# Performance work log

Measured on AMD Instinct MI355X. Metric: run time of the kernel, lower is better.

The kernel has to match this reference:

```python
import jax, jax.numpy as jnp
import numpy as np

N = 100000      # nodes
E = 1600000     # directed edges (before self loops)
IN, H, OUT = 16, 64, 8
NEG_SLOPE = 0.2  # PyG GATConv default


def setup_inputs() -> dict:
    key = jax.random.key(0)
    ks = jax.random.split(key, 12)
    g = lambda k, sh, s: (jax.random.normal(k, sh, dtype=jnp.float32) * s)
    return {
        "x": jax.random.normal(ks[0], (N, IN), dtype=jnp.float32),
        "edge_index": jax.random.randint(ks[1], (2, E), 0, N, dtype=jnp.int32),
        # layer 1 (GATConv: weight, att_src, att_dst, bias)
        "W1": g(ks[2], (IN, H), 1.0 / np.sqrt(IN)),
        "a_src1": g(ks[3], (H,), 0.1),
        "a_dst1": g(ks[4], (H,), 0.1),
        "b1": jnp.zeros((H,), jnp.float32),
        # layer 2
        "W2": g(ks[5], (H, H), 1.0 / np.sqrt(H)),
        "a_src2": g(ks[6], (H,), 0.1),
        "a_dst2": g(ks[7], (H,), 0.1),
        "b2": jnp.zeros((H,), jnp.float32),
        # policy head
        "Wp": g(ks[8], (H, OUT), 1.0 / np.sqrt(H)),
        "bp": jnp.zeros((OUT,), jnp.float32),
    }


def gat_conv(x, src, dst, W, a_src, a_dst, b):
    """PyG GATConv, heads=1: softmax over incoming edges grouped by dst."""
    h = x @ W                                   # [N, H]
    e = (h @ a_src)[src] + (h @ a_dst)[dst]      # [E'] raw attention logits
    e = jnp.where(e > 0, e, NEG_SLOPE * e)       # leaky_relu
    m = jax.ops.segment_max(e, dst, num_segments=N)
    m = jnp.where(jnp.isfinite(m), m, 0.0)       # guard empty segments
    w = jnp.exp(e - m[dst])
    den = jax.ops.segment_sum(w, dst, num_segments=N)
    alpha = w / (den[dst] + 1e-16)               # per-edge softmax weight
    out = jax.ops.segment_sum(h[src] * alpha[:, None], dst, num_segments=N)
    return out + b


def reference(x, edge_index, W1, a_src1, a_dst1, b1, W2, a_src2, a_dst2, b2, Wp, bp):
    # add self loops once (PyG default add_self_loops=True)
    loops = jnp.arange(N, dtype=edge_index.dtype)
    src = jnp.concatenate([edge_index[0], loops])
    dst = jnp.concatenate([edge_index[1], loops])
    h = jax.nn.relu(gat_conv(x, src, dst, W1, a_src1, a_dst1, b1))
    h = jax.nn.relu(gat_conv(h, src, dst, W2, a_src2, a_dst2, b2))
    return h @ Wp + bp  # [N, OUT]
```

## Files before the change

### kernel.cpp

```cpp
#include <hip/hip_runtime.h>
#include <hip/hip_fp16.h>
#include <math.h>

#define NEG_SLOPE 0.2f
#define TILE 2048

__device__ __forceinline__ float wave_reduce_sum(float v){
  #pragma unroll
  for (int off = 32; off > 0; off >>= 1) v += __shfl_xor(v, off, 64);
  return v;
}
__device__ __forceinline__ float wave_reduce_max(float v){
  #pragma unroll
  for (int off = 32; off > 0; off >>= 1) v = fmaxf(v, __shfl_xor(v, off, 64));
  return v;
}


__global__ void k_bcount(const int* __restrict__ ei, int* __restrict__ C,
                         int* __restrict__ Btot, int E, int TOT, int NB, int T){
  __shared__ int hist[512];
  int t = blockIdx.x;
  for (int i = threadIdx.x; i < NB; i += blockDim.x) hist[i] = 0;
  __syncthreads();
  int base = t * TILE;
  for (int k = threadIdx.x; k < TILE; k += blockDim.x){
    int j = base + k;
    if (j < TOT){
      int d = (j < E) ? ei[E + j] : (j - E);
      atomicAdd(&hist[d >> 8], 1);
    }
  }
  __syncthreads();
  for (int b = threadIdx.x; b < NB; b += blockDim.x){
    int v = hist[b];
    C[(size_t)b * T + t] = v;
    if (v) atomicAdd(&Btot[b], v);
  }
}

__global__ void k_bstart(const int* __restrict__ Btot, int* __restrict__ Bstart,
                         int* __restrict__ rowptr, int NB, int TOT, int N){
  __shared__ int lds[512];
  int t = threadIdx.x;
  int total = (t < NB) ? Btot[t] : 0;
  lds[t] = total; __syncthreads();
  for (int off = 1; off < 512; off <<= 1){
    int x = (t >= off) ? lds[t - off] : 0;
    __syncthreads();
    lds[t] += x;
    __syncthreads();
  }
  if (t < NB) Bstart[t] = lds[t] - total;
  if (t == 0){ Bstart[NB] = TOT; rowptr[N] = TOT; }
}

__global__ void k_bcolscan(const int* __restrict__ C, const int* __restrict__ Bstart,
                           int* __restrict__ O, int NB, int T){
  int wid = (blockIdx.x * blockDim.x + threadIdx.x) >> 6;
  int lane = threadIdx.x & 63;
  if (wid >= NB) return;
  int run = Bstart[wid];
  int nchunks = (T + 63) / 64;
  for (int i = 0; i < nchunks; i++){
    int t = i * 64 + lane;
    int v = (t < T) ? C[(size_t)wid * T + t] : 0;
    int s = v;
    #pragma unroll
    for (int off = 1; off < 64; off <<= 1){
      int u = __shfl_up(s, off);
      if (lane >= off) s += u;
    }
    if (t < T) O[(size_t)wid * T + t] = run + (s - v);
    run += __shfl(s, 63);
  }
}

__global__ void k_bscatter(const int* __restrict__ ei, const int* __restrict__ O,
                           unsigned int* __restrict__ tmp, int E, int TOT, int NB, int T){
  __shared__ int cur[512];
  int t = blockIdx.x;
  for (int b = threadIdx.x; b < NB; b += blockDim.x) cur[b] = O[(size_t)b * T + t];
  __syncthreads();
  int base = t * TILE;
  for (int k = threadIdx.x; k < TILE; k += blockDim.x){
    int j = base + k;
    if (j < TOT){
      int s, d;
      if (j < E){ s = ei[j]; d = ei[E + j]; } else { s = j - E; d = s; }
      int r = atomicAdd(&cur[d >> 8], 1);
      tmp[r] = ((unsigned)s << 8) | (unsigned)(d & 255);
    }
  }
}

__global__ void k_bfinal(const unsigned int* __restrict__ tmp, const int* __restrict__ Bstart,
                         int* __restrict__ rowptr, int* __restrict__ col, int N){
  __shared__ int hist[256];
  __shared__ int sc[256];
  __shared__ int cur[256];
  int b = blockIdx.x;
  int base_node = b << 8;
  int nnode = min(256, N - base_node);
  int beg = Bstart[b], end = Bstart[b + 1];
  int t = threadIdx.x;
  if (t < 256) hist[t] = 0;
  __syncthreads();
  for (int j = beg + t; j < end; j += blockDim.x)
    atomicAdd(&hist[tmp[j] & 255u], 1);
  __syncthreads();
  int v = 0;
  if (t < 256){ v = hist[t]; sc[t] = v; }
  __syncthreads();
  for (int off = 1; off < 256; off <<= 1){
    int x = (t < 256 && t >= off) ? sc[t - off] : 0;
    __syncthreads();
    if (t < 256) sc[t] += x;
    __syncthreads();
  }
  if (t < 256){
    int excl = sc[t] - v;
    if (t < nnode) rowptr[base_node + t] = beg + excl;
    cur[t] = beg + excl;
  }
  __syncthreads();
  for (int j = beg + t; j < end; j += blockDim.x){
    unsigned u = tmp[j];
    int pos = atomicAdd(&cur[u & 255u], 1);
    col[pos] = (int)(u >> 8);
  }
}


__global__ void k_dense16(const float* __restrict__ x, const float* __restrict__ W,
                          const float* __restrict__ asrc, const float* __restrict__ adst,
                          __half* __restrict__ h16, float* __restrict__ sarr, float* __restrict__ darr,
                          int n){
  __shared__ float4 Ws4[16 * 16];
  __shared__ float as_s[64], ad_s[64];
  int t = threadIdx.x;
  const float4* W4 = (const float4*)W;
  if (t < 16 * 16) Ws4[t] = W4[t];
  if (t < 64){ as_s[t] = asrc[t]; ad_s[t] = adst[t]; }
  __syncthreads();
  int gid = blockIdx.x * blockDim.x + t;
  int node = gid >> 1;
  int half = gid & 1;
  if (node >= n) return;
  const float4* xr = (const float4*)(x + (size_t)node * 16);
  float4 acc[8] = {};
  #pragma unroll
  for (int kk = 0; kk < 4; kk++){
    float4 xv = xr[kk];
    #pragma unroll
    for (int i = 0; i < 4; i++){
      float xk = (i == 0) ? xv.x : (i == 1) ? xv.y : (i == 2) ? xv.z : xv.w;
      const float4* wrow = &Ws4[(kk * 4 + i) * 16 + half * 8];
      #pragma unroll
      for (int c = 0; c < 8; c++){
        acc[c].x = fmaf(xk, wrow[c].x, acc[c].x);
        acc[c].y = fmaf(xk, wrow[c].y, acc[c].y);
        acc[c].z = fmaf(xk, wrow[c].z, acc[c].z);
        acc[c].w = fmaf(xk, wrow[c].w, acc[c].w);
      }
    }
  }
  float sv = 0.f, dv = 0.f;
  #pragma unroll
  for (int c = 0; c < 8; c += 2){
    union { __half2 h2[4]; uint4 u; } pk;
    pk.h2[0] = __floats2half2_rn(acc[c].x,   acc[c].y);
    pk.h2[1] = __floats2half2_rn(acc[c].z,   acc[c].w);
    pk.h2[2] = __floats2half2_rn(acc[c+1].x, acc[c+1].y);
    pk.h2[3] = __floats2half2_rn(acc[c+1].z, acc[c+1].w);
    *(uint4*)(h16 + (size_t)node * 64 + half * 32 + c * 4) = pk.u;
  }
  #pragma unroll
  for (int c = 0; c < 8; c++){
    int cb = half * 32 + c * 4;
    sv += acc[c].x * as_s[cb] + acc[c].y * as_s[cb+1] + acc[c].z * as_s[cb+2] + acc[c].w * as_s[cb+3];
    dv += acc[c].x * ad_s[cb] + acc[c].y * ad_s[cb+1] + acc[c].z * ad_s[cb+2] + acc[c].w * ad_s[cb+3];
  }
  sv += __shfl_xor(sv, 1);
  dv += __shfl_xor(dv, 1);
  if (half == 0){ sarr[node] = sv; darr[node] = dv; }
}

__global__ void k_dense64(const float* __restrict__ x, const float* __restrict__ W,
                          const float* __restrict__ asrc, const float* __restrict__ adst,
                          __half* __restrict__ h16, float* __restrict__ sarr, float* __restrict__ darr,
                          int n){
  __shared__ float4 Ws4[64 * 16];
  __shared__ float as_s[64], ad_s[64];
  int t = threadIdx.x;
  const float4* W4 = (const float4*)W;
  for (int i = t; i < 64 * 16; i += blockDim.x) Ws4[i] = W4[i];
  if (t < 64){ as_s[t] = asrc[t]; ad_s[t] = adst[t]; }
  __syncthreads();
  int gid = blockIdx.x * blockDim.x + t;
  int node = gid >> 1;
  int half = gid & 1;
  if (node >= n) return;
  const float4* xr = (const float4*)(x + (size_t)node * 64);
  float4 acc[8] = {};
  #pragma unroll
  for (int kk = 0; kk < 16; kk++){
    float4 xv = xr[kk];
    #pragma unroll
    for (int i = 0; i < 4; i++){
      float xk = (i == 0) ? xv.x : (i == 1) ? xv.y : (i == 2) ? xv.z : xv.w;
      const float4* wrow = &Ws4[(kk * 4 + i) * 16 + half * 8];
      #pragma unroll
      for (int c = 0; c < 8; c++){
        acc[c].x = fmaf(xk, wrow[c].x, acc[c].x);
        acc[c].y = fmaf(xk, wrow[c].y, acc[c].y);
        acc[c].z = fmaf(xk, wrow[c].z, acc[c].z);
        acc[c].w = fmaf(xk, wrow[c].w, acc[c].w);
      }
    }
  }
  float sv = 0.f, dv = 0.f;
  #pragma unroll
  for (int c = 0; c < 8; c += 2){
    union { __half2 h2[4]; uint4 u; } pk;
    pk.h2[0] = __floats2half2_rn(acc[c].x,   acc[c].y);
    pk.h2[1] = __floats2half2_rn(acc[c].z,   acc[c].w);
    pk.h2[2] = __floats2half2_rn(acc[c+1].x, acc[c+1].y);
    pk.h2[3] = __floats2half2_rn(acc[c+1].z, acc[c+1].w);
    *(uint4*)(h16 + (size_t)node * 64 + half * 32 + c * 4) = pk.u;
  }
  #pragma unroll
  for (int c = 0; c < 8; c++){
    int cb = half * 32 + c * 4;
    sv += acc[c].x * as_s[cb] + acc[c].y * as_s[cb+1] + acc[c].z * as_s[cb+2] + acc[c].w * as_s[cb+3];
    dv += acc[c].x * ad_s[cb] + acc[c].y * ad_s[cb+1] + acc[c].z * ad_s[cb+2] + acc[c].w * ad_s[cb+3];
  }
  sv += __shfl_xor(sv, 1);
  dv += __shfl_xor(dv, 1);
  if (half == 0){ sarr[node] = sv; darr[node] = dv; }
}


__device__ __forceinline__ void agg_softmax(const float* sarr, const int* col,
                                            int beg, int deg, float dn, int lane,
                                            int& c0, int& c1, float& a0, float& a1){
  c0 = 0; c1 = 0;
  float e0 = -INFINITY, e1 = -INFINITY;
  if (lane < deg){
    c0 = col[beg + lane];
    float t = sarr[c0] + dn;
    e0 = (t > 0.f) ? t : NEG_SLOPE * t;
  }
  if (lane + 64 < deg){
    c1 = col[beg + lane + 64];
    float t = sarr[c1] + dn;
    e1 = (t > 0.f) ? t : NEG_SLOPE * t;
  }
  float m = wave_reduce_max(fmaxf(e0, e1));
  float w0 = (lane < deg)      ? __expf(e0 - m) : 0.f;
  float w1 = (lane + 64 < deg) ? __expf(e1 - m) : 0.f;
  float sum = wave_reduce_sum(w0 + w1);
  float inv = 1.f / (sum + 1e-16f);
  a0 = w0 * inv; a1 = w1 * inv;
}

__device__ __forceinline__ void agg_gather16(const __half* h16, int deg, int lane,
                                             const int2* stash, float4& A0, float4& A1){
  int eg = lane & 7, co = lane >> 3;
  float4 a0v = make_float4(0.f,0.f,0.f,0.f), a1v = make_float4(0.f,0.f,0.f,0.f);
  #pragma unroll 2
  for (int j0 = 0; j0 < deg; j0 += 8){
    int idx = j0 + eg;
    if (idx < deg){
      int2 ca = stash[idx];
      float a = __int_as_float(ca.y);
      uint4 raw = *(const uint4*)(h16 + (size_t)ca.x * 64 + co * 8);
      float2 f0 = __half22float2(*(__half2*)&raw.x);
      float2 f1 = __half22float2(*(__half2*)&raw.y);
      float2 f2 = __half22float2(*(__half2*)&raw.z);
      float2 f3 = __half22float2(*(__half2*)&raw.w);
      a0v.x = fmaf(a, f0.x, a0v.x); a0v.y = fmaf(a, f0.y, a0v.y);
      a0v.z = fmaf(a, f1.x, a0v.z); a0v.w = fmaf(a, f1.y, a0v.w);
      a1v.x = fmaf(a, f2.x, a1v.x); a1v.y = fmaf(a, f2.y, a1v.y);
      a1v.z = fmaf(a, f3.x, a1v.z); a1v.w = fmaf(a, f3.y, a1v.w);
    }
  }
  #pragma unroll
  for (int off = 1; off < 8; off <<= 1){
    a0v.x += __shfl_xor(a0v.x, off); a0v.y += __shfl_xor(a0v.y, off);
    a0v.z += __shfl_xor(a0v.z, off); a0v.w += __shfl_xor(a0v.w, off);
    a1v.x += __shfl_xor(a1v.x, off); a1v.y += __shfl_xor(a1v.y, off);
    a1v.z += __shfl_xor(a1v.z, off); a1v.w += __shfl_xor(a1v.w, off);
  }
  A0 = a0v; A1 = a1v;
}

__global__ void k_agg1(const __half* __restrict__ h16, const float* __restrict__ sarr,
                       const float* __restrict__ darr, const int* __restrict__ rowptr,
                       const int* __restrict__ col, const float* __restrict__ bias,
                       float* __restrict__ out, int n){
  __shared__ int2 stash[4][128];
  int w = threadIdx.x >> 6;
  int lane = threadIdx.x & 63;
  int node = blockIdx.x * (blockDim.x >> 6) + w;
  if (node >= n) return;
  int beg = rowptr[node];
  int deg = rowptr[node + 1] - beg;
  float dn = darr[node];

  if (deg <= 128){
    int c0, c1; float a0, a1;
    agg_softmax(sarr, col, beg, deg, dn, lane, c0, c1, a0, a1);
    if (lane < deg)      stash[w][lane]      = make_int2(c0, __float_as_int(a0));
    if (lane + 64 < deg) stash[w][lane + 64] = make_int2(c1, __float_as_int(a1));
    float4 A0, A1;
    agg_gather16(h16, deg, lane, stash[w], A0, A1);
    int eg = lane & 7, co = lane >> 3;
    if (eg == 0){
      const float4 b0 = *(const float4*)(bias + co * 8);
      const float4 b1 = *(const float4*)(bias + co * 8 + 4);
      float4 r0, r1;
      r0.x = fmaxf(A0.x + b0.x, 0.f); r0.y = fmaxf(A0.y + b0.y, 0.f);
      r0.z = fmaxf(A0.z + b0.z, 0.f); r0.w = fmaxf(A0.w + b0.w, 0.f);
      r1.x = fmaxf(A1.x + b1.x, 0.f); r1.y = fmaxf(A1.y + b1.y, 0.f);
      r1.z = fmaxf(A1.z + b1.z, 0.f); r1.w = fmaxf(A1.w + b1.w, 0.f);
      *(float4*)(out + (size_t)node * 64 + co * 8)     = r0;
      *(float4*)(out + (size_t)node * 64 + co * 8 + 4) = r1;
    }
  } else {
    float m = -INFINITY;
    int end = beg + deg;
    for (int j = beg + lane; j < end; j += 64){
      float e = sarr[col[j]] + dn;
      e = (e > 0.f) ? e : NEG_SLOPE * e;
      m = fmaxf(m, e);
    }
    m = wave_reduce_max(m);
    float sum = 0.f;
    for (int j = beg + lane; j < end; j += 64){
      float e = sarr[col[j]] + dn;
      e = (e > 0.f) ? e : NEG_SLOPE * e;
      sum += __expf(e - m);
    }
    sum = wave_reduce_sum(sum);
    float invden = 1.0f / (sum + 1e-16f);
    float acc = 0.f;
    for (int j = beg; j < end; j++){
      int s = col[j];
      float e = sarr[s] + dn;
      e = (e > 0.f) ? e : NEG_SLOPE * e;
      float alpha = __expf(e - m) * invden;
      acc = fmaf(alpha, __half2float(h16[(size_t)s * 64 + lane]), acc);
    }
    float r = acc + bias[lane];
    out[(size_t)node * 64 + lane] = fmaxf(r, 0.f);
  }
}

__global__ void k_agg2(const __half* __restrict__ h16, const float* __restrict__ sarr,
                       const float* __restrict__ darr, const int* __restrict__ rowptr,
                       const int* __restrict__ col, const float* __restrict__ bias,
                       const float* __restrict__ Wp, const float* __restrict__ bp,
                       float* __restrict__ out, int n){
  __shared__ int2 stash[4][128];
  int w = threadIdx.x >> 6;
  int lane = threadIdx.x & 63;
  int o = lane & 7, g = lane >> 3;
  float wp[8];
  #pragma unroll
  for (int j = 0; j < 8; j++) wp[j] = Wp[(g * 8 + j) * 8 + o];
  float bpv = bp[o];

  int node = blockIdx.x * (blockDim.x >> 6) + w;
  if (node >= n) return;
  int beg = rowptr[node];
  int deg = rowptr[node + 1] - beg;
  float dn = darr[node];

  if (deg <= 128){
    int c0, c1; float a0, a1;
    agg_softmax(sarr, col, beg, deg, dn, lane, c0, c1, a0, a1);
    if (lane < deg)      stash[w][lane]      = make_int2(c0, __float_as_int(a0));
    if (lane + 64 < deg) stash[w][lane + 64] = make_int2(c1, __float_as_int(a1));
    float4 A0, A1;
    agg_gather16(h16, deg, lane, stash[w], A0, A1);
    const float4 b0 = *(const float4*)(bias + g * 8);
    const float4 b1 = *(const float4*)(bias + g * 8 + 4);
    float r0 = fmaxf(A0.x + b0.x, 0.f), r1 = fmaxf(A0.y + b0.y, 0.f);
    float r2 = fmaxf(A0.z + b0.z, 0.f), r3 = fmaxf(A0.w + b0.w, 0.f);
    float r4 = fmaxf(A1.x + b1.x, 0.f), r5 = fmaxf(A1.y + b1.y, 0.f);
    float r6 = fmaxf(A1.z + b1.z, 0.f), r7 = fmaxf(A1.w + b1.w, 0.f);
    float po = r0*wp[0] + r1*wp[1] + r2*wp[2] + r3*wp[3]
             + r4*wp[4] + r5*wp[5] + r6*wp[6] + r7*wp[7];
    po += __shfl_xor(po, 8);
    po += __shfl_xor(po, 16);
    po += __shfl_xor(po, 32);
    if (lane < 8) out[(size_t)node * 8 + lane] = po + bpv;
  } else {
    int end = beg + deg;
    float m = -INFINITY;
    for (int j = beg + lane; j < end; j += 64){
      float e = sarr[col[j]] + dn;
      e = (e > 0.f) ? e : NEG_SLOPE * e;
      m = fmaxf(m, e);
    }
    m = wave_reduce_max(m);
    float sum = 0.f;
    for (int j = beg + lane; j < end; j += 64){
      float e = sarr[col[j]] + dn;
      e = (e > 0.f) ? e : NEG_SLOPE * e;
      sum += __expf(e - m);
    }
    sum = wave_reduce_sum(sum);
    float invden = 1.0f / (sum + 1e-16f);
    float acc = 0.f;
    for (int j = beg; j < end; j++){
      int s = col[j];
      float e = sarr[s] + dn;
      e = (e > 0.f) ? e : NEG_SLOPE * e;
      float alpha = __expf(e - m) * invden;
      acc = fmaf(alpha, __half2float(h16[(size_t)s * 64 + lane]), acc);
    }
    float r = fmaxf(acc + bias[lane], 0.f);
    float po = 0.f;
    #pragma unroll
    for (int j = 0; j < 8; j++) po += __shfl(r, g * 8 + j) * wp[j];
    po += __shfl_xor(po, 8);
    po += __shfl_xor(po, 16);
    po += __shfl_xor(po, 32);
    if (lane < 8) out[(size_t)node * 8 + lane] = po + bpv;
  }
}


extern "C" void kernel_launch(void* const* d_in, const int* in_sizes, int n_in,
                              void* d_out, int out_size, void* d_ws, size_t ws_size,
                              hipStream_t stream) {
  const float* x   = (const float*)d_in[0];
  const int*   ei  = (const int*)  d_in[1];
  const float* W1  = (const float*)d_in[2];
  const float* as1 = (const float*)d_in[3];
  const float* ad1 = (const float*)d_in[4];
  const float* b1  = (const float*)d_in[5];
  const float* W2  = (const float*)d_in[6];
  const float* as2 = (const float*)d_in[7];
  const float* ad2 = (const float*)d_in[8];
  const float* b2  = (const float*)d_in[9];
  const float* Wp  = (const float*)d_in[10];
  const float* bp  = (const float*)d_in[11];
  float* out = (float*)d_out;

  int N = in_sizes[0] / 16;
  int E = in_sizes[1] / 2;
  int TOT = E + N;
  int NB = (N + 255) >> 8;
  int T  = (TOT + TILE - 1) / TILE;

  char* p = (char*)d_ws;
  auto alloc = [&](size_t bytes) -> char* {
    char* r = p; p += (bytes + 255) & ~(size_t)255; return r;
  };
  __half* h16   = (__half*)alloc((size_t)N * 64 * 2);
  float* buf    = (float*)alloc((size_t)N * 64 * 4);
  float* sA     = (float*)alloc((size_t)N * 4);
  float* dA     = (float*)alloc((size_t)N * 4);
  int*   rowptr = (int*)  alloc((size_t)(N + 1) * 4);
  int*   col    = (int*)  alloc((size_t)TOT * 4);
  int*   Bstart = (int*)  alloc((size_t)(NB + 1) * 4);
  int*   Btot   = (int*)  alloc((size_t)(NB + 1) * 4);

  unsigned int* tmp  = (unsigned int*)h16;
  int*          Cmat = (int*)buf;
  int*          Omat = Cmat + (size_t)NB * T;

  const int tb = 256;

  (void)hipMemsetAsync(Btot, 0, (size_t)(NB + 1) * 4, stream);
  k_bcount<<<T, tb, 0, stream>>>(ei, Cmat, Btot, E, TOT, NB, T);
  k_bstart<<<1, 512, 0, stream>>>(Btot, Bstart, rowptr, NB, TOT, N);
  k_bcolscan<<<(NB + 3) / 4, tb, 0, stream>>>(Cmat, Bstart, Omat, NB, T);
  k_bscatter<<<T, tb, 0, stream>>>(ei, Omat, tmp, E, TOT, NB, T);
  k_bfinal<<<NB, 512, 0, stream>>>(tmp, Bstart, rowptr, col, N);

  k_dense16<<<(2 * N + tb - 1) / tb, tb, 0, stream>>>(x, W1, as1, ad1, h16, sA, dA, N);
  k_agg1<<<(N + 3) / 4, 256, 0, stream>>>(h16, sA, dA, rowptr, col, b1, buf, N);
  k_dense64<<<(2 * N + tb - 1) / tb, tb, 0, stream>>>(buf, W2, as2, ad2, h16, sA, dA, N);
  k_agg2<<<(N + 3) / 4, 256, 0, stream>>>(h16, sA, dA, rowptr, col, b2, Wp, bp, out, N);
}
```

Before: 232.6 us.

## Fuse layer-2 dense projection into layer-1 aggregation with persistent grid

Folds the 64x64 W2 projection and the attention-score dot products into the first aggregation kernel. It also switches that kernel to a grid-stride loop over 2048 blocks that each load W2 into shared memory once. This removes the fp32 intermediate buffer write/read and one kernel launch, and writes fp16 features plus the score arrays into separate buffers. The bucket-sort TILE also grows, cutting the number of count/scatter tiles. The cost is more per-node shuffle-reduction work, 16KB of shared memory per block that may limit occupancy, and fp16 rounding of the projected layer-2 features.

```diff
diff --git a/kernel.cpp b/kernel.cpp
--- a/kernel.cpp
+++ b/kernel.cpp
@@ -3,7 +3,7 @@
 #include <math.h>
 
 #define NEG_SLOPE 0.2f
-#define TILE 2048
+#define TILE 8192
 
 __device__ __forceinline__ float wave_reduce_sum(float v){
   #pragma unroll
@@ -151,60 +151,6 @@
   float4 acc[8] = {};
   #pragma unroll
   for (int kk = 0; kk < 4; kk++){
-    float4 xv = xr[kk];
-    #pragma unroll
-    for (int i = 0; i < 4; i++){
-      float xk = (i == 0) ? xv.x : (i == 1) ? xv.y : (i == 2) ? xv.z : xv.w;
-      const float4* wrow = &Ws4[(kk * 4 + i) * 16 + half * 8];
-      #pragma unroll
-      for (int c = 0; c < 8; c++){
-        acc[c].x = fmaf(xk, wrow[c].x, acc[c].x);
-        acc[c].y = fmaf(xk, wrow[c].y, acc[c].y);
-        acc[c].z = fmaf(xk, wrow[c].z, acc[c].z);
-        acc[c].w = fmaf(xk, wrow[c].w, acc[c].w);
-      }
-    }
-  }
-  float sv = 0.f, dv = 0.f;
-  #pragma unroll
-  for (int c = 0; c < 8; c += 2){
-    union { __half2 h2[4]; uint4 u; } pk;
-    pk.h2[0] = __floats2half2_rn(acc[c].x,   acc[c].y);
-    pk.h2[1] = __floats2half2_rn(acc[c].z,   acc[c].w);
-    pk.h2[2] = __floats2half2_rn(acc[c+1].x, acc[c+1].y);
-    pk.h2[3] = __floats2half2_rn(acc[c+1].z, acc[c+1].w);
-    *(uint4*)(h16 + (size_t)node * 64 + half * 32 + c * 4) = pk.u;
-  }
-  #pragma unroll
-  for (int c = 0; c < 8; c++){
-    int cb = half * 32 + c * 4;
-    sv += acc[c].x * as_s[cb] + acc[c].y * as_s[cb+1] + acc[c].z * as_s[cb+2] + acc[c].w * as_s[cb+3];
-    dv += acc[c].x * ad_s[cb] + acc[c].y * ad_s[cb+1] + acc[c].z * ad_s[cb+2] + acc[c].w * ad_s[cb+3];
-  }
-  sv += __shfl_xor(sv, 1);
-  dv += __shfl_xor(dv, 1);
-  if (half == 0){ sarr[node] = sv; darr[node] = dv; }
-}
-
-__global__ void k_dense64(const float* __restrict__ x, const float* __restrict__ W,
-                          const float* __restrict__ asrc, const float* __restrict__ adst,
-                          __half* __restrict__ h16, float* __restrict__ sarr, float* __restrict__ darr,
-                          int n){
-  __shared__ float4 Ws4[64 * 16];
-  __shared__ float as_s[64], ad_s[64];
-  int t = threadIdx.x;
-  const float4* W4 = (const float4*)W;
-  for (int i = t; i < 64 * 16; i += blockDim.x) Ws4[i] = W4[i];
-  if (t < 64){ as_s[t] = asrc[t]; ad_s[t] = adst[t]; }
-  __syncthreads();
-  int gid = blockIdx.x * blockDim.x + t;
-  int node = gid >> 1;
-  int half = gid & 1;
-  if (node >= n) return;
-  const float4* xr = (const float4*)(x + (size_t)node * 64);
-  float4 acc[8] = {};
-  #pragma unroll
-  for (int kk = 0; kk < 16; kk++){
     float4 xv = xr[kk];
     #pragma unroll
     for (int i = 0; i < 4; i++){
@@ -295,65 +241,105 @@
   A0 = a0v; A1 = a1v;
 }
 
-__global__ void k_agg1(const __half* __restrict__ h16, const float* __restrict__ sarr,
-                       const float* __restrict__ darr, const int* __restrict__ rowptr,
-                       const int* __restrict__ col, const float* __restrict__ bias,
-                       float* __restrict__ out, int n){
+__global__ void k_agg1f(const __half* __restrict__ h16, const float* __restrict__ sarr,
+                        const float* __restrict__ darr, const int* __restrict__ rowptr,
+                        const int* __restrict__ col, const float* __restrict__ b1,
+                        const float* __restrict__ W2, const float* __restrict__ as2,
+                        const float* __restrict__ ad2,
+                        __half* __restrict__ g16, float* __restrict__ sB, float* __restrict__ dB,
+                        int n){
   __shared__ int2 stash[4][128];
-  int w = threadIdx.x >> 6;
-  int lane = threadIdx.x & 63;
-  int node = blockIdx.x * (blockDim.x >> 6) + w;
-  if (node >= n) return;
-  int beg = rowptr[node];
-  int deg = rowptr[node + 1] - beg;
-  float dn = darr[node];
-
-  if (deg <= 128){
-    int c0, c1; float a0, a1;
-    agg_softmax(sarr, col, beg, deg, dn, lane, c0, c1, a0, a1);
-    if (lane < deg)      stash[w][lane]      = make_int2(c0, __float_as_int(a0));
-    if (lane + 64 < deg) stash[w][lane + 64] = make_int2(c1, __float_as_int(a1));
-    float4 A0, A1;
-    agg_gather16(h16, deg, lane, stash[w], A0, A1);
-    int eg = lane & 7, co = lane >> 3;
-    if (eg == 0){
-      const float4 b0 = *(const float4*)(bias + co * 8);
-      const float4 b1 = *(const float4*)(bias + co * 8 + 4);
-      float4 r0, r1;
-      r0.x = fmaxf(A0.x + b0.x, 0.f); r0.y = fmaxf(A0.y + b0.y, 0.f);
-      r0.z = fmaxf(A0.z + b0.z, 0.f); r0.w = fmaxf(A0.w + b0.w, 0.f);
-      r1.x = fmaxf(A1.x + b1.x, 0.f); r1.y = fmaxf(A1.y + b1.y, 0.f);
-      r1.z = fmaxf(A1.z + b1.z, 0.f); r1.w = fmaxf(A1.w + b1.w, 0.f);
-      *(float4*)(out + (size_t)node * 64 + co * 8)     = r0;
-      *(float4*)(out + (size_t)node * 64 + co * 8 + 4) = r1;
-    }
-  } else {
-    float m = -INFINITY;
-    int end = beg + deg;
-    for (int j = beg + lane; j < end; j += 64){
-      float e = sarr[col[j]] + dn;
-      e = (e > 0.f) ? e : NEG_SLOPE * e;
-      m = fmaxf(m, e);
-    }
-    m = wave_reduce_max(m);
-    float sum = 0.f;
-    for (int j = beg + lane; j < end; j += 64){
-      float e = sarr[col[j]] + dn;
-      e = (e > 0.f) ? e : NEG_SLOPE * e;
-      sum += __expf(e - m);
-    }
-    sum = wave_reduce_sum(sum);
-    float invden = 1.0f / (sum + 1e-16f);
-    float acc = 0.f;
-    for (int j = beg; j < end; j++){
-      int s = col[j];
-      float e = sarr[s] + dn;
-      e = (e > 0.f) ? e : NEG_SLOPE * e;
-      float alpha = __expf(e - m) * invden;
-      acc = fmaf(alpha, __half2float(h16[(size_t)s * 64 + lane]), acc);
-    }
-    float r = acc + bias[lane];
-    out[(size_t)node * 64 + lane] = fmaxf(r, 0.f);
+  __shared__ float W2s[64 * 64];
+  __shared__ float as_s[64], ad_s[64];
+  int t = threadIdx.x;
+  for (int i = t; i < 4096; i += 256)
+    W2s[(i & 63) * 64 + (i >> 6)] = W2[i];
+  if (t < 64){ as_s[t] = as2[t]; ad_s[t] = ad2[t]; }
+  __syncthreads();
+
+  int w = t >> 6, lane = t & 63;
+  int eg = lane & 7, co = lane >> 3;
+  int stride = gridDim.x * 4;
+
+  for (int node = blockIdx.x * 4 + w; node < n; node += stride){
+    int beg = rowptr[node];
+    int deg = rowptr[node + 1] - beg;
+    float dn = darr[node];
+    float r[8];
+
+    if (deg <= 128){
+      int c0, c1; float a0, a1;
+      agg_softmax(sarr, col, beg, deg, dn, lane, c0, c1, a0, a1);
+      if (lane < deg)      stash[w][lane]      = make_int2(c0, __float_as_int(a0));
+      if (lane + 64 < deg) stash[w][lane + 64] = make_int2(c1, __float_as_int(a1));
+      float4 A0, A1;
+      agg_gather16(h16, deg, lane, stash[w], A0, A1);
+      const float4 b0 = *(const float4*)(b1 + co * 8);
+      const float4 b1v = *(const float4*)(b1 + co * 8 + 4);
+      r[0] = fmaxf(A0.x + b0.x, 0.f);  r[1] = fmaxf(A0.y + b0.y, 0.f);
+      r[2] = fmaxf(A0.z + b0.z, 0.f);  r[3] = fmaxf(A0.w + b0.w, 0.f);
+      r[4] = fmaxf(A1.x + b1v.x, 0.f); r[5] = fmaxf(A1.y + b1v.y, 0.f);
+      r[6] = fmaxf(A1.z + b1v.z, 0.f); r[7] = fmaxf(A1.w + b1v.w, 0.f);
+    } else {
+      int end = beg + deg;
+      float m = -INFINITY;
+      for (int j = beg + lane; j < end; j += 64){
+        float e = sarr[col[j]] + dn;
+        e = (e > 0.f) ? e : NEG_SLOPE * e;
+        m = fmaxf(m, e);
+      }
+      m = wave_reduce_max(m);
+      float sum = 0.f;
+      for (int j = beg + lane; j < end; j += 64){
+        float e = sarr[col[j]] + dn;
+        e = (e > 0.f) ? e : NEG_SLOPE * e;
+        sum += __expf(e - m);
+      }
+      sum = wave_reduce_sum(sum);
+      float invden = 1.0f / (sum + 1e-16f);
+      float acc = 0.f;
+      for (int j = beg; j < end; j++){
+        int s = col[j];
+        float e = sarr[s] + dn;
+        e = (e > 0.f) ? e : NEG_SLOPE * e;
+        float alpha = __expf(e - m) * invden;
+        acc = fmaf(alpha, __half2float(h16[(size_t)s * 64 + lane]), acc);
+      }
+      float rs = fmaxf(acc + b1[lane], 0.f);
+      #pragma unroll
+      for (int i = 0; i < 8; i++) r[i] = __shfl(rs, co * 8 + i);
+    }
+
+    float po[8];
+    #pragma unroll
+    for (int j = 0; j < 8; j++){
+      const float4* row = (const float4*)(W2s + (eg * 8 + j) * 64 + co * 8);
+      float4 wa = row[0], wb = row[1];
+      po[j] = r[0]*wa.x + r[1]*wa.y + r[2]*wa.z + r[3]*wa.w
+            + r[4]*wb.x + r[5]*wb.y + r[6]*wb.z + r[7]*wb.w;
+    }
+    #pragma unroll
+    for (int off = 8; off < 64; off <<= 1){
+      #pragma unroll
+      for (int j = 0; j < 8; j++) po[j] += __shfl_xor(po[j], off);
+    }
+    if (co == 0){
+      union { __half2 h2[4]; uint4 u; } pk;
+      pk.h2[0] = __floats2half2_rn(po[0], po[1]);
+      pk.h2[1] = __floats2half2_rn(po[2], po[3]);
+      pk.h2[2] = __floats2half2_rn(po[4], po[5]);
+      pk.h2[3] = __floats2half2_rn(po[6], po[7]);
+      *(uint4*)(g16 + (size_t)node * 64 + eg * 8) = pk.u;
+    }
+    float sv = 0.f, dv = 0.f;
+    #pragma unroll
+    for (int j = 0; j < 8; j++){
+      sv += po[j] * as_s[eg * 8 + j];
+      dv += po[j] * ad_s[eg * 8 + j];
+    }
+    sv += __shfl_xor(sv, 1); sv += __shfl_xor(sv, 2); sv += __shfl_xor(sv, 4);
+    dv += __shfl_xor(dv, 1); dv += __shfl_xor(dv, 2); dv += __shfl_xor(dv, 4);
+    if (lane == 0){ sB[node] = sv; dB[node] = dv; }
   }
 }
 
@@ -461,16 +447,18 @@
     char* r = p; p += (bytes + 255) & ~(size_t)255; return r;
   };
   __half* h16   = (__half*)alloc((size_t)N * 64 * 2);
-  float* buf    = (float*)alloc((size_t)N * 64 * 4);
+  __half* g16   = (__half*)alloc((size_t)N * 64 * 2);
   float* sA     = (float*)alloc((size_t)N * 4);
   float* dA     = (float*)alloc((size_t)N * 4);
+  float* sB     = (float*)alloc((size_t)N * 4);
+  float* dB     = (float*)alloc((size_t)N * 4);
   int*   rowptr = (int*)  alloc((size_t)(N + 1) * 4);
   int*   col    = (int*)  alloc((size_t)TOT * 4);
   int*   Bstart = (int*)  alloc((size_t)(NB + 1) * 4);
   int*   Btot   = (int*)  alloc((size_t)(NB + 1) * 4);
 
   unsigned int* tmp  = (unsigned int*)h16;
-  int*          Cmat = (int*)buf;
+  int*          Cmat = (int*)g16;
   int*          Omat = Cmat + (size_t)NB * T;
 
   const int tb = 256;
@@ -483,7 +471,8 @@
   k_bfinal<<<NB, 512, 0, stream>>>(tmp, Bstart, rowptr, col, N);
 
   k_dense16<<<(2 * N + tb - 1) / tb, tb, 0, stream>>>(x, W1, as1, ad1, h16, sA, dA, N);
-  k_agg1<<<(N + 3) / 4, 256, 0, stream>>>(h16, sA, dA, rowptr, col, b1, buf, N);
-  k_dense64<<<(2 * N + tb - 1) / tb, tb, 0, stream>>>(buf, W2, as2, ad2, h16, sA, dA, N);
-  k_agg2<<<(N + 3) / 4, 256, 0, stream>>>(h16, sA, dA, rowptr, col, b2, Wp, bp, out, N);
-}
+  int g1blocks = 2048;
+  k_agg1f<<<g1blocks, 256, 0, stream>>>(h16, sA, dA, rowptr, col, b1,
+                                        W2, as2, ad2, g16, sB, dB, N);
+  k_agg2<<<(N + 3) / 4, 256, 0, stream>>>(g16, sB, dB, rowptr, col, b2, Wp, bp, out, N);
+}
```

After: 286.6 us. 23.2% more time.
